# Kernel tuning notes

Hardware: AMD Instinct MI355X
Metric: run time of the kernel (lower is better)

## Reference

```python
import jax, jax.numpy as jnp
import numpy as np
from jax import lax


def setup_inputs() -> dict:
    key = jax.random.key(0)
    k1, k2, k3 = jax.random.split(key, 3)
    B, P, D = 4, 64, 768
    N, R = 2048, 12
    positions = jax.random.normal(k1, (B, P, D), dtype=jnp.float32)
    # module inits keys with std=0.01 (we use randn*0.01); adjacency is a learned
    # dense R x N x N parameter (init zeros in source -> use small noise so the
    # read path is non-degenerate for kernel correctness checks)
    keys_param = jax.random.normal(k2, (N, D), dtype=jnp.float32) * 0.01
    adjacency = jax.random.normal(k3, (R, N, N), dtype=jnp.float32) * 0.01
    return {"positions": positions, "keys_param": keys_param,
            "adjacency": adjacency, "k": 16}


def reference(positions, keys_param, adjacency, k):
    # keys property: L2-normalize along feature dim
    keys = keys_param * lax.rsqrt(
        jnp.sum(keys_param * keys_param, axis=-1, keepdims=True) + 1e-12)

    # anchor: key matching scores = positions . keys^T  -> (B, P, N)
    scores = jnp.einsum('bpd,nd->bpn', positions, keys)

    # topk_sparse addressing: keep top-k nodes per position, normalize to sum 1
    vals, idx = lax.top_k(scores, k)           # (B, P, k)
    w = jax.nn.softmax(vals, axis=-1)          # normalized anchor weights

    # read: position -> node -> (rel, nei_node), honoring top-k sparsity by
    # gathering only the k selected adjacency rows per relation (no dense BPN matmul)
    adj_rows = adjacency[:, idx, :]            # (R, B, P, k, N) gather
    nei = jnp.einsum('bpk,rbpkn->bpn', w, adj_rows)   # neighbor node scores

    # project neighbor node distribution back through keys -> (B, P, D)
    out = jnp.einsum('bpn,nd->bpd', nei, keys)
    return out
```

## Files before the change

### kernel.cpp

```cpp
#include <hip/hip_runtime.h>
#include <math.h>

#define B_ 4
#define P_ 64
#define D_ 768
#define N_ 2048
#define R_ 12
#define K_ 16
#define Q_ 256
#define SSPLIT_ 4
#define SPLITS_ 16
#define BK_ 32
#define NEG_INF_ -3.0e38f

__global__ __launch_bounds__(256) void k_front(const float* __restrict__ pos,
                                               const float* __restrict__ kp,
                                               const float* __restrict__ adj,
                                               float* __restrict__ spart,
                                               float* __restrict__ keys,
                                               float* __restrict__ invn,
                                               float* __restrict__ asum) {
    __shared__ float Ast[BK_][68];
    __shared__ float Bst[BK_][68];
    int bid = blockIdx.x;
    int tid = threadIdx.x;
    if (bid < 512) {
        int z = bid >> 7;
        int t = bid & 127;
        int n0 = (t & 31) * 64, q0 = (t >> 5) * 64;
        int tx = tid & 15, ty = tid >> 4;
        float acc[4][4] = {};
        for (int kb = z * (D_ / SSPLIT_); kb < (z + 1) * (D_ / SSPLIT_); kb += BK_) {
            #pragma unroll
            for (int e = 0; e < 2; e++) {
                int elem = tid + e * 256;
                int row = elem >> 3, c4 = elem & 7;
                float4 v = *(const float4*)(pos + (size_t)(q0 + row) * D_ + kb + c4 * 4);
                Ast[c4 * 4 + 0][row] = v.x; Ast[c4 * 4 + 1][row] = v.y;
                Ast[c4 * 4 + 2][row] = v.z; Ast[c4 * 4 + 3][row] = v.w;
            }
            #pragma unroll
            for (int e = 0; e < 2; e++) {
                int elem = tid + e * 256;
                int row = elem >> 3, c4 = elem & 7;
                float4 v = *(const float4*)(kp + (size_t)(n0 + row) * D_ + kb + c4 * 4);
                Bst[c4 * 4 + 0][row] = v.x; Bst[c4 * 4 + 1][row] = v.y;
                Bst[c4 * 4 + 2][row] = v.z; Bst[c4 * 4 + 3][row] = v.w;
            }
            __syncthreads();
            #pragma unroll 4
            for (int kk = 0; kk < BK_; kk++) {
                float4 a = *(const float4*)&Ast[kk][ty * 4];
                float4 b = *(const float4*)&Bst[kk][tx * 4];
                float av[4] = {a.x, a.y, a.z, a.w};
                float bv[4] = {b.x, b.y, b.z, b.w};
                #pragma unroll
                for (int i = 0; i < 4; i++)
                    #pragma unroll
                    for (int j = 0; j < 4; j++)
                        acc[i][j] += av[i] * bv[j];
            }
            __syncthreads();
        }
        float* base = spart + (size_t)z * Q_ * N_;
        #pragma unroll
        for (int i = 0; i < 4; i++) {
            float4 v = {acc[i][0], acc[i][1], acc[i][2], acc[i][3]};
            *(float4*)(base + (size_t)(q0 + ty * 4 + i) * N_ + n0 + tx * 4) = v;
        }
    } else if (bid < 1024) {
        int row = (bid - 512) * 4 + (tid >> 6);
        int lane = tid & 63;
        const float4* src = (const float4*)(kp + (size_t)row * D_);
        float4 a = src[lane], b = src[lane + 64], c = src[lane + 128];
        float ss = a.x * a.x + a.y * a.y + a.z * a.z + a.w * a.w
                 + b.x * b.x + b.y * b.y + b.z * b.z + b.w * b.w
                 + c.x * c.x + c.y * c.y + c.z * c.z + c.w * c.w;
        #pragma unroll
        for (int off = 32; off > 0; off >>= 1) ss += __shfl_down(ss, off, 64);
        ss = __shfl(ss, 0, 64);
        float inv = 1.0f / sqrtf(ss + 1e-12f);
        float4* dst = (float4*)(keys + (size_t)row * D_);
        float4 oa = {a.x * inv, a.y * inv, a.z * inv, a.w * inv};
        float4 ob = {b.x * inv, b.y * inv, b.z * inv, b.w * inv};
        float4 oc = {c.x * inv, c.y * inv, c.z * inv, c.w * inv};
        dst[lane] = oa; dst[lane + 64] = ob; dst[lane + 128] = oc;
        if (lane == 0) invn[row] = inv;
    } else {
        size_t i = (size_t)(bid - 1024) * 256 + tid;
        const float4* a4 = (const float4*)adj;
        const size_t plane = (size_t)N_ * N_ / 4;
        float4 acc = {0.f, 0.f, 0.f, 0.f};
        #pragma unroll
        for (int r = 0; r < R_; r++) {
            float4 v = a4[(size_t)r * plane + i];
            acc.x += v.x; acc.y += v.y; acc.z += v.z; acc.w += v.w;
        }
        ((float4*)asum)[i] = acc;
    }
}

__global__ __launch_bounds__(256) void k_topk_nei(const float* __restrict__ spart,
                                                  const float* __restrict__ invn,
                                                  const float* __restrict__ asum,
                                                  float* __restrict__ nei) {
    int q = blockIdx.x, tid = threadIdx.x;
    int w = tid >> 6, lane = tid & 63;
    int base = w * 512 + lane;
    const float* r0 = spart + (size_t)q * N_;
    const size_t pl = (size_t)Q_ * N_;
    float v[8];
    #pragma unroll
    for (int j = 0; j < 8; j++) {
        int n = base + j * 64;
        v[j] = (r0[n] + r0[pl + n] + r0[2 * pl + n] + r0[3 * pl + n]) * invn[n];
    }
    __shared__ float cv[64];
    __shared__ int ci[64];
    __shared__ float sw[K_];
    __shared__ int si[K_];
    for (int r = 0; r < K_; r++) {
        float bv = NEG_INF_;
        int bi = 0;
        #pragma unroll
        for (int j = 0; j < 8; j++) {
            int n = base + j * 64;
            if (v[j] > bv) { bv = v[j]; bi = n; }
        }
        #pragma unroll
        for (int off = 1; off < 64; off <<= 1) {
            float ov = __shfl_xor(bv, off, 64);
            int oi = __shfl_xor(bi, off, 64);
            if (ov > bv || (ov == bv && oi < bi)) { bv = ov; bi = oi; }
        }
        if (lane == 0) { cv[w * K_ + r] = bv; ci[w * K_ + r] = bi; }
        #pragma unroll
        for (int j = 0; j < 8; j++)
            if (base + j * 64 == bi) v[j] = NEG_INF_;
    }
    __syncthreads();
    if (w == 0) {
        float mv = cv[lane];
        int mi = ci[lane];
        float sel_v = NEG_INF_;
        int sel_i = 0;
        for (int r = 0; r < K_; r++) {
            float bv = mv;
            int bi = mi;
            #pragma unroll
            for (int off = 1; off < 64; off <<= 1) {
                float ov = __shfl_xor(bv, off, 64);
                int oi = __shfl_xor(bi, off, 64);
                if (ov > bv || (ov == bv && oi < bi)) { bv = ov; bi = oi; }
            }
            if (lane == r) { sel_v = bv; sel_i = bi; }
            if (mi == bi) mv = NEG_INF_;
        }
        float m = __shfl(sel_v, 0, 64);
        float e = (lane < K_) ? expf(sel_v - m) : 0.0f;
        float sum = e;
        #pragma unroll
        for (int off = 1; off < 64; off <<= 1) sum += __shfl_xor(sum, off, 64);
        if (lane < K_) { sw[lane] = e / sum; si[lane] = sel_i; }
    }
    __syncthreads();
    float4 acc0 = {0.f, 0.f, 0.f, 0.f};
    float4 acc1 = {0.f, 0.f, 0.f, 0.f};
    #pragma unroll
    for (int k = 0; k < K_; k++) {
        const float4* row = (const float4*)(asum + (size_t)si[k] * N_);
        float wk = sw[k];
        float4 v0 = row[tid], v1 = row[tid + 256];
        acc0.x += wk * v0.x; acc0.y += wk * v0.y; acc0.z += wk * v0.z; acc0.w += wk * v0.w;
        acc1.x += wk * v1.x; acc1.y += wk * v1.y; acc1.z += wk * v1.z; acc1.w += wk * v1.w;
    }
    float4* dst = (float4*)(nei + (size_t)q * N_);
    dst[tid] = acc0;
    dst[tid + 256] = acc1;
}

__global__ __launch_bounds__(256) void k_out_part(const float* __restrict__ nei,
                                                  const float* __restrict__ keys,
                                                  float* __restrict__ part) {
    __shared__ float Ast[BK_][68];
    __shared__ float Bst[BK_][68];
    int tid = threadIdx.x;
    int tx = tid & 15, ty = tid >> 4;
    int d0 = blockIdx.x * 64;
    int q0 = blockIdx.y * 64;
    int z = blockIdx.z;
    float acc[4][4] = {};
    for (int kb = z * (N_ / SPLITS_); kb < (z + 1) * (N_ / SPLITS_); kb += BK_) {
        #pragma unroll
        for (int e = 0; e < 2; e++) {
            int elem = tid + e * 256;
            int row = elem >> 3, c4 = elem & 7;
            float4 v = *(const float4*)(nei + (size_t)(q0 + row) * N_ + kb + c4 * 4);
            Ast[c4 * 4 + 0][row] = v.x; Ast[c4 * 4 + 1][row] = v.y;
            Ast[c4 * 4 + 2][row] = v.z; Ast[c4 * 4 + 3][row] = v.w;
        }
        #pragma unroll
        for (int e = 0; e < 2; e++) {
            int elem = tid + e * 256;
            int kr = elem >> 4, c4 = elem & 15;
            float4 v = *(const float4*)(keys + (size_t)(kb + kr) * D_ + d0 + c4 * 4);
            *(float4*)&Bst[kr][c4 * 4] = v;
        }
        __syncthreads();
        #pragma unroll 4
        for (int kk = 0; kk < BK_; kk++) {
            float4 a = *(const float4*)&Ast[kk][ty * 4];
            float4 b = *(const float4*)&Bst[kk][tx * 4];
            float av[4] = {a.x, a.y, a.z, a.w};
            float bv[4] = {b.x, b.y, b.z, b.w};
            #pragma unroll
            for (int i = 0; i < 4; i++)
                #pragma unroll
                for (int j = 0; j < 4; j++)
                    acc[i][j] += av[i] * bv[j];
        }
        __syncthreads();
    }
    float* base = part + (size_t)z * Q_ * D_;
    #pragma unroll
    for (int i = 0; i < 4; i++) {
        float4 v = {acc[i][0], acc[i][1], acc[i][2], acc[i][3]};
        *(float4*)(base + (size_t)(q0 + ty * 4 + i) * D_ + d0 + tx * 4) = v;
    }
}

__global__ __launch_bounds__(256) void k_reduce(const float* __restrict__ part,
                                                float* __restrict__ out) {
    int i = blockIdx.x * 256 + threadIdx.x;
    const float4* p4 = (const float4*)part;
    const int plane = Q_ * D_ / 4;
    float4 acc = {0.f, 0.f, 0.f, 0.f};
    #pragma unroll
    for (int z = 0; z < SPLITS_; z++) {
        float4 v = p4[(size_t)z * plane + i];
        acc.x += v.x; acc.y += v.y; acc.z += v.z; acc.w += v.w;
    }
    ((float4*)out)[i] = acc;
}

extern "C" void kernel_launch(void* const* d_in, const int* in_sizes, int n_in,
                              void* d_out, int out_size, void* d_ws, size_t ws_size,
                              hipStream_t stream) {
    const float* pos = (const float*)d_in[0];
    const float* kp  = (const float*)d_in[1];
    const float* adj = (const float*)d_in[2];
    float* out = (float*)d_out;

    float* ws     = (float*)d_ws;
    float* keys   = ws;
    float* invn   = keys + (size_t)N_ * D_;
    float* asum   = invn + N_;
    float* spart  = asum + (size_t)N_ * N_;
    float* nei    = spart + (size_t)SSPLIT_ * Q_ * N_;
    float* part   = asum;

    k_front<<<5120, 256, 0, stream>>>(pos, kp, adj, spart, keys, invn, asum);
    k_topk_nei<<<Q_, 256, 0, stream>>>(spart, invn, asum, nei);
    k_out_part<<<dim3(12, 4, SPLITS_), 256, 0, stream>>>(nei, keys, part);
    k_reduce<<<192, 256, 0, stream>>>(part, out);
}
```

Before: 340.5 us.

## Fuse all stages into one persistent kernel with grid-wide barriers

Replaces the four separate launches with a single persistent kernel of 768 blocks. Phases are separated by atomic-counter grid barriers, and the counters are cleared by a memset before launch. The adjacency relation-sum now uses a grid-stride loop, and the top-k/neighbor stage is split across two blocks per query so more CUs do work. The goal is to remove launch gaps and tail idle time between stages. In exchange it adds barrier spin cost, redundant top-k work in the paired blocks, and depends on all 768 blocks being resident at once to avoid deadlock.

```diff
diff --git a/kernel.cpp b/kernel.cpp
--- a/kernel.cpp
+++ b/kernel.cpp
@@ -11,19 +11,38 @@
 #define SSPLIT_ 4
 #define SPLITS_ 16
 #define BK_ 32
+#define GRID_ 768
 #define NEG_INF_ -3.0e38f
 
-__global__ __launch_bounds__(256) void k_front(const float* __restrict__ pos,
-                                               const float* __restrict__ kp,
-                                               const float* __restrict__ adj,
-                                               float* __restrict__ spart,
-                                               float* __restrict__ keys,
-                                               float* __restrict__ invn,
-                                               float* __restrict__ asum) {
+__device__ __forceinline__ void grid_barrier(int* cnt) {
+    __syncthreads();
+    if (threadIdx.x == 0) {
+        __threadfence();
+        __hip_atomic_fetch_add(cnt, 1, __ATOMIC_RELAXED, __HIP_MEMORY_SCOPE_AGENT);
+        while (__hip_atomic_load(cnt, __ATOMIC_RELAXED, __HIP_MEMORY_SCOPE_AGENT) < GRID_)
+            __builtin_amdgcn_s_sleep(1);
+        __threadfence();
+    }
+    __syncthreads();
+}
+
+__global__ __launch_bounds__(256, 3) void k_mega(
+        const float* __restrict__ pos, const float* __restrict__ kp,
+        const float* __restrict__ adj, float* __restrict__ spart,
+        float* __restrict__ keys, float* __restrict__ invn,
+        float* __restrict__ asum, float* __restrict__ nei,
+        float* __restrict__ part, float* __restrict__ out,
+        int* __restrict__ bar) {
     __shared__ float Ast[BK_][68];
     __shared__ float Bst[BK_][68];
+    __shared__ float cv[64];
+    __shared__ int ci[64];
+    __shared__ float sw[K_];
+    __shared__ int si[K_];
+
     int bid = blockIdx.x;
     int tid = threadIdx.x;
+
     if (bid < 512) {
         int z = bid >> 7;
         int t = bid & 127;
@@ -68,8 +87,9 @@
             float4 v = {acc[i][0], acc[i][1], acc[i][2], acc[i][3]};
             *(float4*)(base + (size_t)(q0 + ty * 4 + i) * N_ + n0 + tx * 4) = v;
         }
-    } else if (bid < 1024) {
-        int row = (bid - 512) * 4 + (tid >> 6);
+    }
+    if (bid >= 256) {
+        int row = (bid - 256) * 4 + (tid >> 6);
         int lane = tid & 63;
         const float4* src = (const float4*)(kp + (size_t)row * D_);
         float4 a = src[lane], b = src[lane + 64], c = src[lane + 128];
@@ -86,161 +106,152 @@
         float4 oc = {c.x * inv, c.y * inv, c.z * inv, c.w * inv};
         dst[lane] = oa; dst[lane + 64] = ob; dst[lane + 128] = oc;
         if (lane == 0) invn[row] = inv;
-    } else {
-        size_t i = (size_t)(bid - 1024) * 256 + tid;
+    }
+    {
         const float4* a4 = (const float4*)adj;
         const size_t plane = (size_t)N_ * N_ / 4;
-        float4 acc = {0.f, 0.f, 0.f, 0.f};
-        #pragma unroll
-        for (int r = 0; r < R_; r++) {
-            float4 v = a4[(size_t)r * plane + i];
-            acc.x += v.x; acc.y += v.y; acc.z += v.z; acc.w += v.w;
-        }
-        ((float4*)asum)[i] = acc;
-    }
-}
-
-__global__ __launch_bounds__(256) void k_topk_nei(const float* __restrict__ spart,
-                                                  const float* __restrict__ invn,
-                                                  const float* __restrict__ asum,
-                                                  float* __restrict__ nei) {
-    int q = blockIdx.x, tid = threadIdx.x;
-    int w = tid >> 6, lane = tid & 63;
-    int base = w * 512 + lane;
-    const float* r0 = spart + (size_t)q * N_;
-    const size_t pl = (size_t)Q_ * N_;
-    float v[8];
-    #pragma unroll
-    for (int j = 0; j < 8; j++) {
-        int n = base + j * 64;
-        v[j] = (r0[n] + r0[pl + n] + r0[2 * pl + n] + r0[3 * pl + n]) * invn[n];
-    }
-    __shared__ float cv[64];
-    __shared__ int ci[64];
-    __shared__ float sw[K_];
-    __shared__ int si[K_];
-    for (int r = 0; r < K_; r++) {
-        float bv = NEG_INF_;
-        int bi = 0;
+        for (int c = bid; c < 4096; c += GRID_) {
+            size_t i = (size_t)c * 256 + tid;
+            float4 acc = {0.f, 0.f, 0.f, 0.f};
+            #pragma unroll
+            for (int r = 0; r < R_; r++) {
+                float4 v = a4[(size_t)r * plane + i];
+                acc.x += v.x; acc.y += v.y; acc.z += v.z; acc.w += v.w;
+            }
+            ((float4*)asum)[i] = acc;
+        }
+    }
+    grid_barrier(bar + 0);
+
+    if (bid < 2 * Q_) {
+        int q = bid >> 1, half = bid & 1;
+        int w = tid >> 6, lane = tid & 63;
+        int base = w * 512 + lane;
+        const float* r0 = spart + (size_t)q * N_;
+        const size_t pl = (size_t)Q_ * N_;
+        float v[8];
         #pragma unroll
         for (int j = 0; j < 8; j++) {
             int n = base + j * 64;
-            if (v[j] > bv) { bv = v[j]; bi = n; }
-        }
-        #pragma unroll
-        for (int off = 1; off < 64; off <<= 1) {
-            float ov = __shfl_xor(bv, off, 64);
-            int oi = __shfl_xor(bi, off, 64);
-            if (ov > bv || (ov == bv && oi < bi)) { bv = ov; bi = oi; }
-        }
-        if (lane == 0) { cv[w * K_ + r] = bv; ci[w * K_ + r] = bi; }
-        #pragma unroll
-        for (int j = 0; j < 8; j++)
-            if (base + j * 64 == bi) v[j] = NEG_INF_;
-    }
-    __syncthreads();
-    if (w == 0) {
-        float mv = cv[lane];
-        int mi = ci[lane];
-        float sel_v = NEG_INF_;
-        int sel_i = 0;
+            v[j] = (r0[n] + r0[pl + n] + r0[2 * pl + n] + r0[3 * pl + n]) * invn[n];
+        }
         for (int r = 0; r < K_; r++) {
-            float bv = mv;
-            int bi = mi;
+            float bv = NEG_INF_;
+            int bi = 0;
+            #pragma unroll
+            for (int j = 0; j < 8; j++) {
+                int n = base + j * 64;
+                if (v[j] > bv) { bv = v[j]; bi = n; }
+            }
             #pragma unroll
             for (int off = 1; off < 64; off <<= 1) {
                 float ov = __shfl_xor(bv, off, 64);
                 int oi = __shfl_xor(bi, off, 64);
                 if (ov > bv || (ov == bv && oi < bi)) { bv = ov; bi = oi; }
             }
-            if (lane == r) { sel_v = bv; sel_i = bi; }
-            if (mi == bi) mv = NEG_INF_;
-        }
-        float m = __shfl(sel_v, 0, 64);
-        float e = (lane < K_) ? expf(sel_v - m) : 0.0f;
-        float sum = e;
-        #pragma unroll
-        for (int off = 1; off < 64; off <<= 1) sum += __shfl_xor(sum, off, 64);
-        if (lane < K_) { sw[lane] = e / sum; si[lane] = sel_i; }
-    }
-    __syncthreads();
-    float4 acc0 = {0.f, 0.f, 0.f, 0.f};
-    float4 acc1 = {0.f, 0.f, 0.f, 0.f};
-    #pragma unroll
-    for (int k = 0; k < K_; k++) {
-        const float4* row = (const float4*)(asum + (size_t)si[k] * N_);
-        float wk = sw[k];
-        float4 v0 = row[tid], v1 = row[tid + 256];
-        acc0.x += wk * v0.x; acc0.y += wk * v0.y; acc0.z += wk * v0.z; acc0.w += wk * v0.w;
-        acc1.x += wk * v1.x; acc1.y += wk * v1.y; acc1.z += wk * v1.z; acc1.w += wk * v1.w;
-    }
-    float4* dst = (float4*)(nei + (size_t)q * N_);
-    dst[tid] = acc0;
-    dst[tid + 256] = acc1;
-}
-
-__global__ __launch_bounds__(256) void k_out_part(const float* __restrict__ nei,
-                                                  const float* __restrict__ keys,
-                                                  float* __restrict__ part) {
-    __shared__ float Ast[BK_][68];
-    __shared__ float Bst[BK_][68];
-    int tid = threadIdx.x;
-    int tx = tid & 15, ty = tid >> 4;
-    int d0 = blockIdx.x * 64;
-    int q0 = blockIdx.y * 64;
-    int z = blockIdx.z;
-    float acc[4][4] = {};
-    for (int kb = z * (N_ / SPLITS_); kb < (z + 1) * (N_ / SPLITS_); kb += BK_) {
-        #pragma unroll
-        for (int e = 0; e < 2; e++) {
-            int elem = tid + e * 256;
-            int row = elem >> 3, c4 = elem & 7;
-            float4 v = *(const float4*)(nei + (size_t)(q0 + row) * N_ + kb + c4 * 4);
-            Ast[c4 * 4 + 0][row] = v.x; Ast[c4 * 4 + 1][row] = v.y;
-            Ast[c4 * 4 + 2][row] = v.z; Ast[c4 * 4 + 3][row] = v.w;
-        }
-        #pragma unroll
-        for (int e = 0; e < 2; e++) {
-            int elem = tid + e * 256;
-            int kr = elem >> 4, c4 = elem & 15;
-            float4 v = *(const float4*)(keys + (size_t)(kb + kr) * D_ + d0 + c4 * 4);
-            *(float4*)&Bst[kr][c4 * 4] = v;
+            if (lane == 0) { cv[w * K_ + r] = bv; ci[w * K_ + r] = bi; }
+            #pragma unroll
+            for (int j = 0; j < 8; j++)
+                if (base + j * 64 == bi) v[j] = NEG_INF_;
         }
         __syncthreads();
-        #pragma unroll 4
-        for (int kk = 0; kk < BK_; kk++) {
-            float4 a = *(const float4*)&Ast[kk][ty * 4];
-            float4 b = *(const float4*)&Bst[kk][tx * 4];
-            float av[4] = {a.x, a.y, a.z, a.w};
-            float bv[4] = {b.x, b.y, b.z, b.w};
-            #pragma unroll
-            for (int i = 0; i < 4; i++)
+        if (w == 0) {
+            float mv = cv[lane];
+            int mi = ci[lane];
+            float sel_v = NEG_INF_;
+            int sel_i = 0;
+            for (int r = 0; r < K_; r++) {
+                float bv = mv;
+                int bi = mi;
                 #pragma unroll
-                for (int j = 0; j < 4; j++)
-                    acc[i][j] += av[i] * bv[j];
+                for (int off = 1; off < 64; off <<= 1) {
+                    float ov = __shfl_xor(bv, off, 64);
+                    int oi = __shfl_xor(bi, off, 64);
+                    if (ov > bv || (ov == bv && oi < bi)) { bv = ov; bi = oi; }
+                }
+                if (lane == r) { sel_v = bv; sel_i = bi; }
+                if (mi == bi) mv = NEG_INF_;
+            }
+            float m = __shfl(sel_v, 0, 64);
+            float e = (lane < K_) ? expf(sel_v - m) : 0.0f;
+            float sum = e;
+            #pragma unroll
+            for (int off = 1; off < 64; off <<= 1) sum += __shfl_xor(sum, off, 64);
+            if (lane < K_) { sw[lane] = e / sum; si[lane] = sel_i; }
         }
         __syncthreads();
-    }
-    float* base = part + (size_t)z * Q_ * D_;
-    #pragma unroll
-    for (int i = 0; i < 4; i++) {
-        float4 v = {acc[i][0], acc[i][1], acc[i][2], acc[i][3]};
-        *(float4*)(base + (size_t)(q0 + ty * 4 + i) * D_ + d0 + tx * 4) = v;
-    }
-}
-
-__global__ __launch_bounds__(256) void k_reduce(const float* __restrict__ part,
-                                                float* __restrict__ out) {
-    int i = blockIdx.x * 256 + threadIdx.x;
-    const float4* p4 = (const float4*)part;
-    const int plane = Q_ * D_ / 4;
-    float4 acc = {0.f, 0.f, 0.f, 0.f};
-    #pragma unroll
-    for (int z = 0; z < SPLITS_; z++) {
-        float4 v = p4[(size_t)z * plane + i];
-        acc.x += v.x; acc.y += v.y; acc.z += v.z; acc.w += v.w;
-    }
-    ((float4*)out)[i] = acc;
+        int off4 = half * (N_ / 2 / 4) + tid;
+        float4 acc0 = {0.f, 0.f, 0.f, 0.f};
+        #pragma unroll
+        for (int k = 0; k < K_; k++) {
+            const float4* row = (const float4*)(asum + (size_t)si[k] * N_);
+            float wk = sw[k];
+            float4 v0 = row[off4];
+            acc0.x += wk * v0.x; acc0.y += wk * v0.y; acc0.z += wk * v0.z; acc0.w += wk * v0.w;
+        }
+        ((float4*)(nei + (size_t)q * N_))[off4] = acc0;
+    }
+    grid_barrier(bar + 1);
+
+    {
+        int t = bid % 48;
+        int z = bid / 48;
+        int d0 = (t % 12) * 64;
+        int q0 = (t / 12) * 64;
+        int tx = tid & 15, ty = tid >> 4;
+        float acc[4][4] = {};
+        for (int kb = z * (N_ / SPLITS_); kb < (z + 1) * (N_ / SPLITS_); kb += BK_) {
+            #pragma unroll
+            for (int e = 0; e < 2; e++) {
+                int elem = tid + e * 256;
+                int row = elem >> 3, c4 = elem & 7;
+                float4 v = *(const float4*)(nei + (size_t)(q0 + row) * N_ + kb + c4 * 4);
+                Ast[c4 * 4 + 0][row] = v.x; Ast[c4 * 4 + 1][row] = v.y;
+                Ast[c4 * 4 + 2][row] = v.z; Ast[c4 * 4 + 3][row] = v.w;
+            }
+            #pragma unroll
+            for (int e = 0; e < 2; e++) {
+                int elem = tid + e * 256;
+                int kr = elem >> 4, c4 = elem & 15;
+                float4 v = *(const float4*)(keys + (size_t)(kb + kr) * D_ + d0 + c4 * 4);
+                *(float4*)&Bst[kr][c4 * 4] = v;
+            }
+            __syncthreads();
+            #pragma unroll 4
+            for (int kk = 0; kk < BK_; kk++) {
+                float4 a = *(const float4*)&Ast[kk][ty * 4];
+                float4 b = *(const float4*)&Bst[kk][tx * 4];
+                float av[4] = {a.x, a.y, a.z, a.w};
+                float bv[4] = {b.x, b.y, b.z, b.w};
+                #pragma unroll
+                for (int i = 0; i < 4; i++)
+                    #pragma unroll
+                    for (int j = 0; j < 4; j++)
+                        acc[i][j] += av[i] * bv[j];
+            }
+            __syncthreads();
+        }
+        float* base = part + (size_t)z * Q_ * D_;
+        #pragma unroll
+        for (int i = 0; i < 4; i++) {
+            float4 v = {acc[i][0], acc[i][1], acc[i][2], acc[i][3]};
+            *(float4*)(base + (size_t)(q0 + ty * 4 + i) * D_ + d0 + tx * 4) = v;
+        }
+    }
+    grid_barrier(bar + 2);
+
+    if (bid < 192) {
+        int i = bid * 256 + tid;
+        const float4* p4 = (const float4*)part;
+        const int plane = Q_ * D_ / 4;
+        float4 acc = {0.f, 0.f, 0.f, 0.f};
+        #pragma unroll
+        for (int z = 0; z < SPLITS_; z++) {
+            float4 v = p4[(size_t)z * plane + i];
+            acc.x += v.x; acc.y += v.y; acc.z += v.z; acc.w += v.w;
+        }
+        ((float4*)out)[i] = acc;
+    }
 }
 
 extern "C" void kernel_launch(void* const* d_in, const int* in_sizes, int n_in,
@@ -257,10 +268,10 @@
     float* asum   = invn + N_;
     float* spart  = asum + (size_t)N_ * N_;
     float* nei    = spart + (size_t)SSPLIT_ * Q_ * N_;
+    int*   bar    = (int*)(nei + (size_t)Q_ * N_);
     float* part   = asum;
 
-    k_front<<<5120, 256, 0, stream>>>(pos, kp, adj, spart, keys, invn, asum);
-    k_topk_nei<<<Q_, 256, 0, stream>>>(spart, invn, asum, nei);
-    k_out_part<<<dim3(12, 4, SPLITS_), 256, 0, stream>>>(nei, keys, part);
-    k_reduce<<<192, 256, 0, stream>>>(part, out);
+    hipMemsetAsync(bar, 0, 128, stream);
+    k_mega<<<GRID_, 256, 0, stream>>>(pos, kp, adj, spart, keys, invn,
+                                      asum, nei, part, out, bar);
 }
```

Result: slower. 595.3 us (+74.9%).

## Fuse split-K reduction into output GEMM and split top-k gather across two blocks

Applied to the files above, without the earlier changes.

The separate reduce kernel is removed. Each output tile now counts finished K-splits with an atomic counter, and the last block to finish sums the partial results and writes the final output. This saves one kernel launch and its global round trip, at the cost of a memset, fences and a serialized tail reduction done by 48 blocks. The top-k/neighbor kernel also runs with twice as many blocks, each writing half of a row. That raises parallelism but repeats the score load and top-k selection in both halves.

```diff
diff --git a/kernel.cpp b/kernel.cpp
--- a/kernel.cpp
+++ b/kernel.cpp
@@ -104,7 +104,8 @@
                                                   const float* __restrict__ invn,
                                                   const float* __restrict__ asum,
                                                   float* __restrict__ nei) {
-    int q = blockIdx.x, tid = threadIdx.x;
+    int bid = blockIdx.x, tid = threadIdx.x;
+    int q = bid >> 1, half = bid & 1;
     int w = tid >> 6, lane = tid & 63;
     int base = w * 512 + lane;
     const float* r0 = spart + (size_t)q * N_;
@@ -164,26 +165,26 @@
         if (lane < K_) { sw[lane] = e / sum; si[lane] = sel_i; }
     }
     __syncthreads();
+    int off4 = half * (N_ / 2 / 4) + tid;
     float4 acc0 = {0.f, 0.f, 0.f, 0.f};
-    float4 acc1 = {0.f, 0.f, 0.f, 0.f};
     #pragma unroll
     for (int k = 0; k < K_; k++) {
         const float4* row = (const float4*)(asum + (size_t)si[k] * N_);
         float wk = sw[k];
-        float4 v0 = row[tid], v1 = row[tid + 256];
+        float4 v0 = row[off4];
         acc0.x += wk * v0.x; acc0.y += wk * v0.y; acc0.z += wk * v0.z; acc0.w += wk * v0.w;
-        acc1.x += wk * v1.x; acc1.y += wk * v1.y; acc1.z += wk * v1.z; acc1.w += wk * v1.w;
-    }
-    float4* dst = (float4*)(nei + (size_t)q * N_);
-    dst[tid] = acc0;
-    dst[tid + 256] = acc1;
-}
-
-__global__ __launch_bounds__(256) void k_out_part(const float* __restrict__ nei,
-                                                  const float* __restrict__ keys,
-                                                  float* __restrict__ part) {
+    }
+    ((float4*)(nei + (size_t)q * N_))[off4] = acc0;
+}
+
+__global__ __launch_bounds__(256) void k_out(const float* __restrict__ nei,
+                                             const float* __restrict__ keys,
+                                             float* __restrict__ part,
+                                             float* __restrict__ out,
+                                             int* __restrict__ done) {
     __shared__ float Ast[BK_][68];
     __shared__ float Bst[BK_][68];
+    __shared__ int sLast;
     int tid = threadIdx.x;
     int tx = tid & 15, ty = tid >> 4;
     int d0 = blockIdx.x * 64;
@@ -227,20 +228,30 @@
         float4 v = {acc[i][0], acc[i][1], acc[i][2], acc[i][3]};
         *(float4*)(base + (size_t)(q0 + ty * 4 + i) * D_ + d0 + tx * 4) = v;
     }
-}
-
-__global__ __launch_bounds__(256) void k_reduce(const float* __restrict__ part,
-                                                float* __restrict__ out) {
-    int i = blockIdx.x * 256 + threadIdx.x;
-    const float4* p4 = (const float4*)part;
-    const int plane = Q_ * D_ / 4;
-    float4 acc = {0.f, 0.f, 0.f, 0.f};
-    #pragma unroll
-    for (int z = 0; z < SPLITS_; z++) {
-        float4 v = p4[(size_t)z * plane + i];
-        acc.x += v.x; acc.y += v.y; acc.z += v.z; acc.w += v.w;
-    }
-    ((float4*)out)[i] = acc;
+    __threadfence();
+    __syncthreads();
+    if (tid == 0) {
+        int old = __hip_atomic_fetch_add(&done[blockIdx.y * 12 + blockIdx.x], 1,
+                                         __ATOMIC_ACQ_REL, __HIP_MEMORY_SCOPE_AGENT);
+        sLast = (old == SPLITS_ - 1);
+    }
+    __syncthreads();
+    if (sLast) {
+        __threadfence();
+        #pragma unroll
+        for (int p = 0; p < 4; p++) {
+            int f = p * 256 + tid;
+            int r = f >> 4, c4 = f & 15;
+            size_t off = (size_t)(q0 + r) * D_ + d0 + c4 * 4;
+            float4 s = {0.f, 0.f, 0.f, 0.f};
+            #pragma unroll
+            for (int zz = 0; zz < SPLITS_; zz++) {
+                float4 v = *(const float4*)(part + (size_t)zz * Q_ * D_ + off);
+                s.x += v.x; s.y += v.y; s.z += v.z; s.w += v.w;
+            }
+            *(float4*)(out + off) = s;
+        }
+    }
 }
 
 extern "C" void kernel_launch(void* const* d_in, const int* in_sizes, int n_in,
@@ -257,10 +268,11 @@
     float* asum   = invn + N_;
     float* spart  = asum + (size_t)N_ * N_;
     float* nei    = spart + (size_t)SSPLIT_ * Q_ * N_;
+    int*   done   = (int*)(nei + (size_t)Q_ * N_);
     float* part   = asum;
 
+    hipMemsetAsync(done, 0, 48 * sizeof(int), stream);
     k_front<<<5120, 256, 0, stream>>>(pos, kp, adj, spart, keys, invn, asum);
-    k_topk_nei<<<Q_, 256, 0, stream>>>(spart, invn, asum, nei);
-    k_out_part<<<dim3(12, 4, SPLITS_), 256, 0, stream>>>(nei, keys, part);
-    k_reduce<<<192, 256, 0, stream>>>(part, out);
-}
+    k_topk_nei<<<2 * Q_, 256, 0, stream>>>(spart, invn, asum, nei);
+    k_out<<<dim3(12, 4, SPLITS_), 256, 0, stream>>>(nei, keys, part, out, done);
+}
```

Result: slower. 453.3 us (+33.2%).
